# Optimization experiments

Hardware: AMD Instinct MI355X
Metric: run time of the kernel (lower is better)

## Reference

```python
import jax, jax.numpy as jnp
import numpy as np

N_HEADS = 16


def setup_inputs() -> dict:
    key = jax.random.key(0)
    ks = jax.random.split(key, 7)
    B, S, D = 2, 2048, 1024
    x = jax.random.normal(ks[0], (B, S, D), dtype=jnp.float32)
    attn_mask = jax.random.normal(ks[1], (S, S), dtype=jnp.float32) * 0.1
    attn_bias = jax.random.normal(ks[2], (B, S, S), dtype=jnp.float32) * 0.1
    Wqkv = jax.random.normal(ks[3], (D, 3 * D), dtype=jnp.float32) * (D ** -0.5)
    bqkv = jnp.zeros((3 * D,), dtype=jnp.float32)
    Wout = jax.random.normal(ks[4], (D, D), dtype=jnp.float32) * (D ** -0.5)
    bout = jnp.zeros((D,), dtype=jnp.float32)
    return {"x": x, "attn_mask": attn_mask, "attn_bias": attn_bias,
            "Wqkv": Wqkv, "bqkv": bqkv, "Wout": Wout, "bout": bout}


def reference(x, attn_mask, attn_bias, Wqkv, bqkv, Wout, bout):
    B, S, D = x.shape
    H = N_HEADS
    hd = D // H
    # qkv projection: [B,S,3D] -> [3,B,H,S,hd]
    qkv = (x @ Wqkv + bqkv).reshape(B, S, 3, H, hd).transpose(2, 0, 3, 1, 4)
    q, k, v = qkv[0], qkv[1], qkv[2]
    scores = jnp.einsum('bhqd,bhkd->bhqk', q, k) / (hd ** 0.5)
    scores = scores + attn_mask[None, None, :, :] + attn_bias[:, None, :, :]
    attn = jax.nn.softmax(scores, axis=-1)  # dropout p=0.0 (eval)
    out = jnp.einsum('bhqk,bhkd->bhqd', attn, v)
    out = out.transpose(0, 2, 1, 3).reshape(B, S, D)
    return out @ Wout + bout
```

## Files before the change

kernel.cpp:

```cpp
#include <hip/hip_runtime.h>
#include <hip/hip_bf16.h>


#define S_LEN 2048
#define DMODEL 1024
#define NH 16
#define HD 64

typedef __bf16 bf16x8 __attribute__((ext_vector_type(8)));
typedef __bf16 bf16x4 __attribute__((ext_vector_type(4)));
typedef __bf16 bf16x2v __attribute__((ext_vector_type(2)));
typedef float f32x4 __attribute__((ext_vector_type(4)));
typedef short s16x4 __attribute__((ext_vector_type(4)));

#define GLD_LDS16(g, l)                                              \
  __builtin_amdgcn_global_load_lds(                                  \
      (const __attribute__((address_space(1))) unsigned int*)(g),    \
      (__attribute__((address_space(3))) unsigned int*)(l), 16, 0, 0)

#if __has_builtin(__builtin_amdgcn_mfma_f32_16x16x16bf16_1k)
#define HAVE_MFMA_16x16x16_BF16 1
#else
#define HAVE_MFMA_16x16x16_BF16 0
#endif

#if __has_builtin(__builtin_amdgcn_exp2f)
#define EXP2F(x) __builtin_amdgcn_exp2f(x)
#else
static __device__ __forceinline__ float EXP2F(float x) {
  float r;
  asm volatile("v_exp_f32 %0, %1" : "=v"(r) : "v"(x));
  return r;
}
#endif

#define LOG2E 1.44269504f

__global__ __launch_bounds__(256) void preprocess(
    const float* __restrict__ x, const float* __restrict__ mask,
    const float* __restrict__ bias, const float* __restrict__ Wqkv,
    const float* __restrict__ Wout, __bf16* __restrict__ Xb,
    __bf16* __restrict__ Wt, __bf16* __restrict__ Wt2,
    __bf16* __restrict__ MB) {
  __shared__ __align__(16) char smem[64 * 65 * 4];
  const int bid = blockIdx.x;
  const int tid = threadIdx.x;

  if (bid < 4096) {
    int i = bid * 256 + tid;
    float4 v = ((const float4*)x)[i];
    bf16x4 o = {(__bf16)v.x, (__bf16)v.y, (__bf16)v.z, (__bf16)v.w};
    *(bf16x4*)&Xb[(size_t)i * 4] = o;
  } else if (bid < 5120) {
    const float* W;
    __bf16* Wo;
    int ncols, n0, k0;
    if (bid < 4864) {
      int id = bid - 4096;
      W = Wqkv; Wo = Wt; ncols = 3072;
      n0 = (id % 48) * 64; k0 = (id / 48) * 64;
    } else {
      int id = bid - 4864;
      W = Wout; Wo = Wt2; ncols = 1024;
      n0 = (id & 15) * 64; k0 = (id >> 4) * 64;
    }
    float(*tile)[65] = (float(*)[65])smem;
    {
      int c = tid & 63, r4 = tid >> 6;
#pragma unroll
      for (int p = 0; p < 16; ++p) {
        int r = r4 + p * 4;
        tile[r][c] = W[(size_t)(k0 + r) * ncols + n0 + c];
      }
    }
    __syncthreads();
    {
      int cc = (tid & 31) * 2, r8 = tid >> 5;
#pragma unroll
      for (int p = 0; p < 8; ++p) {
        int rr = r8 + p * 8;
        bf16x2v o = {(__bf16)tile[cc][rr], (__bf16)tile[cc + 1][rr]};
        *(bf16x2v*)&Wo[(size_t)(n0 + rr) * 1024 + k0 + cc] = o;
      }
    }
  } else {
    int id = bid - 5120;
    const int kt = id & 31, qt = (id >> 5) & 31, b = id >> 10;
    __bf16(*sm)[68] = (__bf16(*)[68])smem;
    {
      const int r0 = tid >> 4;
      const int cc = (tid & 15) * 4;
      const float* mrow = mask + (size_t)(qt * 64) * S_LEN + kt * 64;
      const float* brow =
          bias + ((size_t)b * S_LEN + qt * 64) * S_LEN + kt * 64;
#pragma unroll
      for (int p = 0; p < 4; ++p) {
        int r = r0 + p * 16;
        float4 m = *(const float4*)(mrow + (size_t)r * S_LEN + cc);
        float4 a = *(const float4*)(brow + (size_t)r * S_LEN + cc);
        sm[r][cc + 0] = (__bf16)((m.x + a.x) * LOG2E);
        sm[r][cc + 1] = (__bf16)((m.y + a.y) * LOG2E);
        sm[r][cc + 2] = (__bf16)((m.z + a.z) * LOG2E);
        sm[r][cc + 3] = (__bf16)((m.w + a.w) * LOG2E);
      }
    }
    __syncthreads();
    const int w = tid >> 6, lane = tid & 63;
    const int quad = lane >> 4, cl = lane & 15;
    __bf16 vals[16];
#pragma unroll
    for (int ct = 0; ct < 4; ++ct) {
      bf16x4 v = *(const bf16x4*)&sm[w * 16 + cl][ct * 16 + quad * 4];
      *(bf16x4*)&vals[ct * 4] = v;
    }
    __bf16* op =
        MB + (((size_t)(b * 32 + qt) * 32 + kt) * 4096) + (w * 64 + lane) * 16;
    *(bf16x8*)op = *(bf16x8*)&vals[0];
    *(bf16x8*)(op + 8) = *(bf16x8*)&vals[8];
  }
}

__global__ __launch_bounds__(256) void gemm_qkv_mfma(
    const __bf16* __restrict__ Xb, const __bf16* __restrict__ Wt,
    const float* __restrict__ bqkv, __bf16* __restrict__ Qb,
    __bf16* __restrict__ Kb, __bf16* __restrict__ Vtb) {
  __shared__ __align__(16) __bf16 As[128 * 32];
  __shared__ __align__(16) __bf16 Bs[128 * 32];
  const int tid = threadIdx.x;
  const int w = tid >> 6, lane = tid & 63;
  const int c = lane & 15, quad = lane >> 4;
  const int wm = w >> 1, wn = w & 1;
  const int rowBase = blockIdx.y * 128;
  const int colBase = blockIdx.x * 128;

  f32x4 acc[4][4] = {};

  const __bf16* gA0 =
      Xb + (size_t)(rowBase + w * 32 + (lane >> 2)) * 1024 + (lane & 3) * 8;
  const __bf16* gB0 =
      Wt + (size_t)(colBase + w * 32 + (lane >> 2)) * 1024 + (lane & 3) * 8;
  __bf16* lA0 = &As[(w * 32) * 32];
  __bf16* lB0 = &Bs[(w * 32) * 32];

  for (int k0 = 0; k0 < 1024; k0 += 32) {
    __syncthreads();
#pragma unroll
    for (int p = 0; p < 2; ++p) {
      GLD_LDS16(gA0 + (size_t)p * 16 * 1024 + k0, lA0 + p * 16 * 32);
      GLD_LDS16(gB0 + (size_t)p * 16 * 1024 + k0, lB0 + p * 16 * 32);
    }
    __syncthreads();

    bf16x8 af[4], bfr[4];
#pragma unroll
    for (int mt = 0; mt < 4; ++mt)
      af[mt] = *(const bf16x8*)&As[(wm * 64 + mt * 16 + c) * 32 + quad * 8];
#pragma unroll
    for (int nt = 0; nt < 4; ++nt)
      bfr[nt] = *(const bf16x8*)&Bs[(wn * 64 + nt * 16 + c) * 32 + quad * 8];
#pragma unroll
    for (int mt = 0; mt < 4; ++mt)
#pragma unroll
      for (int nt = 0; nt < 4; ++nt)
        acc[mt][nt] = __builtin_amdgcn_mfma_f32_16x16x32_bf16(
            af[mt], bfr[nt], acc[mt][nt], 0, 0, 0);
  }

#pragma unroll
  for (int mt = 0; mt < 4; ++mt) {
    int row0 = rowBase + wm * 64 + mt * 16 + quad * 4;
#pragma unroll
    for (int nt = 0; nt < 4; ++nt) {
      int col = colBase + wn * 64 + nt * 16 + c;
      float bias = bqkv[col];
      int three = col >> 10;
      int h = (col & 1023) >> 6;
      int d = col & 63;
#pragma unroll
      for (int r = 0; r < 4; ++r) {
        int rr = row0 + r;
        int bb = rr >> 11, s = rr & 2047;
        float val = acc[mt][nt][r] + bias;
        size_t ho = (size_t)(bb * NH + h);
        if (three == 0)
          Qb[(ho * S_LEN + s) * HD + d] = (__bf16)val;
        else if (three == 1)
          Kb[(ho * S_LEN + s) * HD + d] = (__bf16)val;
        else
          Vtb[(ho * HD + d) * S_LEN + s] = (__bf16)val;
      }
    }
  }
}

__global__ __launch_bounds__(256) void attn_mfma(
    const __bf16* __restrict__ Qb, const __bf16* __restrict__ Kb,
    const __bf16* __restrict__ Vtb, const __bf16* __restrict__ MB,
    __bf16* __restrict__ PO, float* __restrict__ L) {
  const int qt = blockIdx.x, h = blockIdx.y;
  const int b = blockIdx.z >> 1, half = blockIdx.z & 1;
  const int kt0 = half * 16;
  const int tid = threadIdx.x;
  const int w = tid >> 6;
  const int lane = tid & 63;
  const int c = lane & 15;
  const int quad = lane >> 4;

  __shared__ __align__(16) __bf16 Ks[2][64 * 64];
  __shared__ __align__(16) __bf16 Vs[2][64 * 64];
#if !HAVE_MFMA_16x16x16_BF16
  __shared__ __align__(16) __bf16 P2[4][16 * 72];
#endif

  const size_t headoff = (size_t)(b * NH + h) * S_LEN * HD;
  const __bf16* Qg = Qb + headoff + (size_t)(qt * 128) * HD;
  const __bf16* Kg = Kb + headoff;
  const __bf16* Vg = Vtb + headoff;
  const __bf16* MBq0 = MB + ((size_t)(b * 32 + qt * 2 + 0) * 32 + kt0) * 4096 +
                       (w * 64 + lane) * 16;
  const __bf16* MBq1 = MB + ((size_t)(b * 32 + qt * 2 + 1) * 32 + kt0) * 4096 +
                       (w * 64 + lane) * 16;

  __bf16* POx = PO + (size_t)half * 4194304;
  float* Lx = L + half * 65536;

  const int f0 = tid >> 3, f1 = f0 + 32;
  const int j = tid & 7;
  const int sj0 = j ^ (f0 & 7);
  const int sj1 = j ^ (f1 & 7);
  const int lds0 = tid * 8;
  const int lds1 = (256 + tid) * 8;

  bf16x8 qa[2][2];
#pragma unroll
  for (int g = 0; g < 2; ++g) {
    qa[g][0] = *(const bf16x8*)(Qg + (g * 64 + w * 16 + c) * HD + quad * 8);
    qa[g][1] =
        *(const bf16x8*)(Qg + (g * 64 + w * 16 + c) * HD + quad * 8 + 32);
  }

  const int rs0 = (quad ^ (c & 7)) * 8;
  const int rs1 = ((quad + 4) ^ (c & 7)) * 8;

  f32x4 Oa[2][4] = {};
  f32x4 psum[2] = {};

  const int kb0 = kt0 * 64;
  GLD_LDS16(Kg + (size_t)(kb0 + f0) * HD + sj0 * 8, &Ks[0][lds0]);
  GLD_LDS16(Kg + (size_t)(kb0 + f1) * HD + sj1 * 8, &Ks[0][lds1]);
  GLD_LDS16(Vg + (size_t)f0 * S_LEN + kb0 + sj0 * 8, &Vs[0][lds0]);
  GLD_LDS16(Vg + (size_t)f1 * S_LEN + kb0 + sj1 * 8, &Vs[0][lds1]);

  const __bf16* kgp0 = Kg + (size_t)(kb0 + 64 + f0) * HD + sj0 * 8;
  const __bf16* kgp1 = Kg + (size_t)(kb0 + 64 + f1) * HD + sj1 * 8;
  const __bf16* vgp0 = Vg + (size_t)f0 * S_LEN + kb0 + 64 + sj0 * 8;
  const __bf16* vgp1 = Vg + (size_t)f1 * S_LEN + kb0 + 64 + sj1 * 8;

  bf16x8 rMB[2][2];
  rMB[0][0] = *(const bf16x8*)MBq0;
  rMB[0][1] = *(const bf16x8*)(MBq0 + 8);
  rMB[1][0] = *(const bf16x8*)MBq1;
  rMB[1][1] = *(const bf16x8*)(MBq1 + 8);

  __syncthreads();

  const float c1 = 0.125f * LOG2E;

#pragma unroll 2
  for (int lkt = 0; lkt < 16; ++lkt) {
    const int cur = lkt & 1, nxt = cur ^ 1;
    bf16x8 nMB[2][2];
    {
      const __bf16* m0 = MBq0 + (size_t)(lkt + 1) * 4096;
      const __bf16* m1 = MBq1 + (size_t)(lkt + 1) * 4096;
      nMB[0][0] = *(const bf16x8*)m0;
      nMB[0][1] = *(const bf16x8*)(m0 + 8);
      nMB[1][0] = *(const bf16x8*)m1;
      nMB[1][1] = *(const bf16x8*)(m1 + 8);
    }
    if (lkt < 15) {
      GLD_LDS16(kgp0, &Ks[nxt][lds0]);
      GLD_LDS16(kgp1, &Ks[nxt][lds1]);
      GLD_LDS16(vgp0, &Vs[nxt][lds0]);
      GLD_LDS16(vgp1, &Vs[nxt][lds1]);
    }
    kgp0 += 64 * HD;
    kgp1 += 64 * HD;
    vgp0 += 64;
    vgp1 += 64;

    bf16x8 kf0[4], kf1[4];
#pragma unroll
    for (int ct = 0; ct < 4; ++ct) {
      kf0[ct] = *(const bf16x8*)&Ks[cur][(ct * 16 + c) * 64 + rs0];
      kf1[ct] = *(const bf16x8*)&Ks[cur][(ct * 16 + c) * 64 + rs1];
    }

    f32x4 sv[2][4];
    __builtin_amdgcn_s_setprio(1);
#pragma unroll
    for (int g = 0; g < 2; ++g)
#pragma unroll
      for (int ct = 0; ct < 4; ++ct) {
        f32x4 a = {};
        a = __builtin_amdgcn_mfma_f32_16x16x32_bf16(kf0[ct], qa[g][0], a, 0,
                                                    0, 0);
        a = __builtin_amdgcn_mfma_f32_16x16x32_bf16(kf1[ct], qa[g][1], a, 0,
                                                    0, 0);
        sv[g][ct] = a;
      }
    __builtin_amdgcn_s_setprio(0);

#if HAVE_MFMA_16x16x16_BF16
    s16x4 vf[4][4];
#pragma unroll
    for (int ft = 0; ft < 4; ++ft) {
      const int fr = ft * 16 + c;
#pragma unroll
      for (int ct = 0; ct < 4; ++ct) {
        const int chunk = ((ct * 2 + (quad >> 1)) ^ (fr & 7)) * 8 +
                          (quad & 1) * 4;
        vf[ft][ct] = *(const s16x4*)&Vs[cur][fr * 64 + chunk];
      }
    }
#endif

    s16x4 pb[2][4];
#pragma unroll
    for (int g = 0; g < 2; ++g)
#pragma unroll
      for (int ct = 0; ct < 4; ++ct) {
        f32x4 pv;
#pragma unroll
        for (int r = 0; r < 4; ++r) {
          float mb = (ct < 2) ? (float)rMB[g][0][ct * 4 + r]
                              : (float)rMB[g][1][(ct - 2) * 4 + r];
          pv[r] = EXP2F(sv[g][ct][r] * c1 + mb);
        }
        psum[g] += pv;
        __bf16 t4[4];
#pragma unroll
        for (int r = 0; r < 4; ++r) t4[r] = (__bf16)pv[r];
        pb[g][ct] = *(s16x4*)t4;
      }
#pragma unroll
    for (int g = 0; g < 2; ++g) {
      rMB[g][0] = nMB[g][0];
      rMB[g][1] = nMB[g][1];
    }

#if HAVE_MFMA_16x16x16_BF16
    __builtin_amdgcn_s_setprio(1);
#pragma unroll
    for (int g = 0; g < 2; ++g)
#pragma unroll
      for (int ft = 0; ft < 4; ++ft)
#pragma unroll
        for (int ct = 0; ct < 4; ++ct)
          Oa[g][ft] = __builtin_amdgcn_mfma_f32_16x16x16bf16_1k(
              vf[ft][ct], pb[g][ct], Oa[g][ft], 0, 0, 0);
    __builtin_amdgcn_s_setprio(0);
#else
#pragma unroll
    for (int g = 0; g < 2; ++g) {
#pragma unroll
      for (int ct = 0; ct < 4; ++ct)
        *(bf16x4*)&P2[w][c * 72 + ct * 16 + quad * 4] = *(bf16x4*)&pb[g][ct];
      bf16x8 pf0 = *(const bf16x8*)&P2[w][c * 72 + quad * 8];
      bf16x8 pf1 = *(const bf16x8*)&P2[w][c * 72 + 32 + quad * 8];
#pragma unroll
      for (int ft = 0; ft < 4; ++ft) {
        const int fr = ft * 16 + c;
        bf16x8 vf0 = *(const bf16x8*)&Vs[cur][fr * 64 + rs0];
        bf16x8 vf1 = *(const bf16x8*)&Vs[cur][fr * 64 + rs1];
        Oa[g][ft] = __builtin_amdgcn_mfma_f32_16x16x32_bf16(vf0, pf0,
                                                            Oa[g][ft], 0, 0, 0);
        Oa[g][ft] = __builtin_amdgcn_mfma_f32_16x16x32_bf16(vf1, pf1,
                                                            Oa[g][ft], 0, 0, 0);
      }
    }
#endif

    __syncthreads();
  }
#pragma unroll
  for (int g = 0; g < 2; ++g) {
    float lsum = psum[g][0] + psum[g][1] + psum[g][2] + psum[g][3];
    lsum += __shfl_xor(lsum, 16);
    lsum += __shfl_xor(lsum, 32);
    if (lane < 16)
      Lx[(size_t)(b * NH + h) * S_LEN + qt * 128 + g * 64 + w * 16 + c] = lsum;
    __bf16* orow = POx +
                   (size_t)(b * S_LEN + qt * 128 + g * 64 + w * 16 + c) *
                       DMODEL +
                   h * HD;
#pragma unroll
    for (int ft = 0; ft < 4; ++ft) {
      __bf16 t4[4];
#pragma unroll
      for (int r = 0; r < 4; ++r) t4[r] = (__bf16)Oa[g][ft][r];
      *(bf16x4*)(orow + ft * 16 + quad * 4) = *(bf16x4*)t4;
    }
  }
}

__global__ __launch_bounds__(256) void combine(const __bf16* __restrict__ PO,
                                               const float* __restrict__ L,
                                               __bf16* __restrict__ AOb) {
  const int i = blockIdx.x * 256 + threadIdx.x;
  const size_t e = (size_t)i * 8;
  const int hidx = (int)(e >> 6) & 15;
  const int s = (int)(e >> 10) & 2047;
  const int b = (int)(e >> 21);
  const size_t li = ((size_t)(b * NH + hidx) << 11) + s;
  const float invl = 1.0f / (L[li] + L[65536 + li]);
  bf16x8 a = *(const bf16x8*)&PO[e];
  bf16x8 c = *(const bf16x8*)&PO[4194304 + e];
  __bf16 o[8];
#pragma unroll
  for (int k = 0; k < 8; ++k)
    o[k] = (__bf16)(((float)a[k] + (float)c[k]) * invl);
  *(bf16x8*)&AOb[e] = *(bf16x8*)o;
}

__global__ __launch_bounds__(256) void gemm_out_mfma(
    const __bf16* __restrict__ AOb, const __bf16* __restrict__ Wt2,
    const float* __restrict__ bout, float* __restrict__ Out) {
  __shared__ __align__(16) __bf16 As[128 * 32];
  __shared__ __align__(16) __bf16 Bs[64 * 32];
  const int tid = threadIdx.x;
  const int w = tid >> 6, lane = tid & 63;
  const int c = lane & 15, quad = lane >> 4;
  const int rowBase = blockIdx.y * 128;
  const int colBase = blockIdx.x * 64;

  f32x4 acc[2][4] = {};

  const __bf16* gA0 =
      AOb + (size_t)(rowBase + w * 32 + (lane >> 2)) * 1024 + (lane & 3) * 8;
  const __bf16* gB0 =
      Wt2 + (size_t)(colBase + w * 16 + (lane >> 2)) * 1024 + (lane & 3) * 8;
  __bf16* lA0 = &As[(w * 32) * 32];
  __bf16* lB0 = &Bs[(w * 16) * 32];

  for (int k0 = 0; k0 < 1024; k0 += 32) {
    __syncthreads();
#pragma unroll
    for (int p = 0; p < 2; ++p)
      GLD_LDS16(gA0 + (size_t)p * 16 * 1024 + k0, lA0 + p * 16 * 32);
    GLD_LDS16(gB0 + k0, lB0);
    __syncthreads();

    bf16x8 af[2], bfr[4];
#pragma unroll
    for (int mt = 0; mt < 2; ++mt)
      af[mt] = *(const bf16x8*)&As[(w * 32 + mt * 16 + c) * 32 + quad * 8];
#pragma unroll
    for (int nt = 0; nt < 4; ++nt)
      bfr[nt] = *(const bf16x8*)&Bs[(nt * 16 + c) * 32 + quad * 8];
#pragma unroll
    for (int mt = 0; mt < 2; ++mt)
#pragma unroll
      for (int nt = 0; nt < 4; ++nt)
        acc[mt][nt] = __builtin_amdgcn_mfma_f32_16x16x32_bf16(
            af[mt], bfr[nt], acc[mt][nt], 0, 0, 0);
  }

#pragma unroll
  for (int mt = 0; mt < 2; ++mt) {
    int row0 = rowBase + w * 32 + mt * 16 + quad * 4;
#pragma unroll
    for (int nt = 0; nt < 4; ++nt) {
      int col = colBase + nt * 16 + c;
      float bias = bout[col];
#pragma unroll
      for (int r = 0; r < 4; ++r)
        Out[(size_t)(row0 + r) * 1024 + col] = acc[mt][nt][r] + bias;
    }
  }
}

extern "C" void kernel_launch(void* const* d_in, const int* in_sizes, int n_in,
                              void* d_out, int out_size, void* d_ws,
                              size_t ws_size, hipStream_t stream) {
  const float* x = (const float*)d_in[0];
  const float* attn_mask = (const float*)d_in[1];
  const float* attn_bias = (const float*)d_in[2];
  const float* Wqkv = (const float*)d_in[3];
  const float* bqkv = (const float*)d_in[4];
  const float* Wout = (const float*)d_in[5];
  const float* bout = (const float*)d_in[6];
  float* out = (float*)d_out;

  __bf16* base = (__bf16*)d_ws;
  __bf16* Xb = base;
  __bf16* PO = base;
  __bf16* Wt = base + 4194304;
  __bf16* Qb = base + 8388608;
  __bf16* Kb = base + 12582912;
  __bf16* Vtb = base + 16777216;
  __bf16* AOb = base + 16777216;
  __bf16* MB = base + 20971520;
  __bf16* Wt2 = base + 29360128;
  float* Lf = (float*)d_out;

  preprocess<<<7168, 256, 0, stream>>>(x, attn_mask, attn_bias, Wqkv, Wout,
                                       Xb, Wt, Wt2, MB);
  gemm_qkv_mfma<<<dim3(24, 32), 256, 0, stream>>>(Xb, Wt, bqkv, Qb, Kb, Vtb);
  attn_mfma<<<dim3(16, NH, 4), 256, 0, stream>>>(Qb, Kb, Vtb, MB, PO, Lf);
  combine<<<2048, 256, 0, stream>>>(PO, Lf, AOb);
  gemm_out_mfma<<<dim3(16, 32), 256, 0, stream>>>(AOb, Wt2, bout, out);
}
```

Before: 278.4 us.

## Drop split-K attention and combine kernel; process 128-key tiles per iteration

The attention kernel no longer splits the key range into two halves. Each block now walks all 32 key tiles as 16 iterations of two 64-key subtiles, with doubled LDS staging, and normalizes the output itself, so the combine kernel and the partial-output/L buffers go away. The preprocess stage also loads each mask tile once and reuses it for both batches, which cuts mask reads and the block count. In exchange the attention grid halves to 512 blocks and LDS per block doubles, which lowers parallelism and occupancy on the GPU.

After: 270.8 us. -2.7%, faster.

```diff
diff --git a/kernel.cpp b/kernel.cpp
--- a/kernel.cpp
+++ b/kernel.cpp
@@ -85,38 +85,42 @@
     }
   } else {
     int id = bid - 5120;
-    const int kt = id & 31, qt = (id >> 5) & 31, b = id >> 10;
+    const int kt = id & 31, qt = id >> 5;
     __bf16(*sm)[68] = (__bf16(*)[68])smem;
-    {
-      const int r0 = tid >> 4;
-      const int cc = (tid & 15) * 4;
-      const float* mrow = mask + (size_t)(qt * 64) * S_LEN + kt * 64;
+    const int r0 = tid >> 4;
+    const int cc = (tid & 15) * 4;
+    const float* mrow = mask + (size_t)(qt * 64) * S_LEN + kt * 64;
+    float4 mld[4];
+#pragma unroll
+    for (int p = 0; p < 4; ++p)
+      mld[p] = *(const float4*)(mrow + (size_t)(r0 + p * 16) * S_LEN + cc);
+    const int w = tid >> 6, lane = tid & 63;
+    const int quad = lane >> 4, cl = lane & 15;
+    for (int b = 0; b < 2; ++b) {
       const float* brow =
           bias + ((size_t)b * S_LEN + qt * 64) * S_LEN + kt * 64;
 #pragma unroll
       for (int p = 0; p < 4; ++p) {
         int r = r0 + p * 16;
-        float4 m = *(const float4*)(mrow + (size_t)r * S_LEN + cc);
         float4 a = *(const float4*)(brow + (size_t)r * S_LEN + cc);
-        sm[r][cc + 0] = (__bf16)((m.x + a.x) * LOG2E);
-        sm[r][cc + 1] = (__bf16)((m.y + a.y) * LOG2E);
-        sm[r][cc + 2] = (__bf16)((m.z + a.z) * LOG2E);
-        sm[r][cc + 3] = (__bf16)((m.w + a.w) * LOG2E);
-      }
-    }
-    __syncthreads();
-    const int w = tid >> 6, lane = tid & 63;
-    const int quad = lane >> 4, cl = lane & 15;
-    __bf16 vals[16];
-#pragma unroll
-    for (int ct = 0; ct < 4; ++ct) {
-      bf16x4 v = *(const bf16x4*)&sm[w * 16 + cl][ct * 16 + quad * 4];
-      *(bf16x4*)&vals[ct * 4] = v;
-    }
-    __bf16* op =
-        MB + (((size_t)(b * 32 + qt) * 32 + kt) * 4096) + (w * 64 + lane) * 16;
-    *(bf16x8*)op = *(bf16x8*)&vals[0];
-    *(bf16x8*)(op + 8) = *(bf16x8*)&vals[8];
+        sm[r][cc + 0] = (__bf16)((mld[p].x + a.x) * LOG2E);
+        sm[r][cc + 1] = (__bf16)((mld[p].y + a.y) * LOG2E);
+        sm[r][cc + 2] = (__bf16)((mld[p].z + a.z) * LOG2E);
+        sm[r][cc + 3] = (__bf16)((mld[p].w + a.w) * LOG2E);
+      }
+      __syncthreads();
+      __bf16 vals[16];
+#pragma unroll
+      for (int ct = 0; ct < 4; ++ct) {
+        bf16x4 v = *(const bf16x4*)&sm[w * 16 + cl][ct * 16 + quad * 4];
+        *(bf16x4*)&vals[ct * 4] = v;
+      }
+      __bf16* op = MB + (((size_t)(b * 32 + qt) * 32 + kt) * 4096) +
+                   (w * 64 + lane) * 16;
+      *(bf16x8*)op = *(bf16x8*)&vals[0];
+      *(bf16x8*)(op + 8) = *(bf16x8*)&vals[8];
+      __syncthreads();
+    }
   }
 }
 
@@ -196,18 +200,16 @@
 __global__ __launch_bounds__(256) void attn_mfma(
     const __bf16* __restrict__ Qb, const __bf16* __restrict__ Kb,
     const __bf16* __restrict__ Vtb, const __bf16* __restrict__ MB,
-    __bf16* __restrict__ PO, float* __restrict__ L) {
-  const int qt = blockIdx.x, h = blockIdx.y;
-  const int b = blockIdx.z >> 1, half = blockIdx.z & 1;
-  const int kt0 = half * 16;
+    __bf16* __restrict__ AOb) {
+  const int qt = blockIdx.x, h = blockIdx.y, b = blockIdx.z;
   const int tid = threadIdx.x;
   const int w = tid >> 6;
   const int lane = tid & 63;
   const int c = lane & 15;
   const int quad = lane >> 4;
 
-  __shared__ __align__(16) __bf16 Ks[2][64 * 64];
-  __shared__ __align__(16) __bf16 Vs[2][64 * 64];
+  __shared__ __align__(16) __bf16 Ks[2][2][64 * 64];
+  __shared__ __align__(16) __bf16 Vs[2][2][64 * 64];
 #if !HAVE_MFMA_16x16x16_BF16
   __shared__ __align__(16) __bf16 P2[4][16 * 72];
 #endif
@@ -216,13 +218,10 @@
   const __bf16* Qg = Qb + headoff + (size_t)(qt * 128) * HD;
   const __bf16* Kg = Kb + headoff;
   const __bf16* Vg = Vtb + headoff;
-  const __bf16* MBq0 = MB + ((size_t)(b * 32 + qt * 2 + 0) * 32 + kt0) * 4096 +
-                       (w * 64 + lane) * 16;
-  const __bf16* MBq1 = MB + ((size_t)(b * 32 + qt * 2 + 1) * 32 + kt0) * 4096 +
-                       (w * 64 + lane) * 16;
-
-  __bf16* POx = PO + (size_t)half * 4194304;
-  float* Lx = L + half * 65536;
+  const __bf16* MBq0 =
+      MB + ((size_t)(b * 32 + qt * 2 + 0) * 32) * 4096 + (w * 64 + lane) * 16;
+  const __bf16* MBq1 =
+      MB + ((size_t)(b * 32 + qt * 2 + 1) * 32) * 4096 + (w * 64 + lane) * 16;
 
   const int f0 = tid >> 3, f1 = f0 + 32;
   const int j = tid & 7;
@@ -245,57 +244,16 @@
   f32x4 Oa[2][4] = {};
   f32x4 psum[2] = {};
 
-  const int kb0 = kt0 * 64;
-  GLD_LDS16(Kg + (size_t)(kb0 + f0) * HD + sj0 * 8, &Ks[0][lds0]);
-  GLD_LDS16(Kg + (size_t)(kb0 + f1) * HD + sj1 * 8, &Ks[0][lds1]);
-  GLD_LDS16(Vg + (size_t)f0 * S_LEN + kb0 + sj0 * 8, &Vs[0][lds0]);
-  GLD_LDS16(Vg + (size_t)f1 * S_LEN + kb0 + sj1 * 8, &Vs[0][lds1]);
-
-  const __bf16* kgp0 = Kg + (size_t)(kb0 + 64 + f0) * HD + sj0 * 8;
-  const __bf16* kgp1 = Kg + (size_t)(kb0 + 64 + f1) * HD + sj1 * 8;
-  const __bf16* vgp0 = Vg + (size_t)f0 * S_LEN + kb0 + 64 + sj0 * 8;
-  const __bf16* vgp1 = Vg + (size_t)f1 * S_LEN + kb0 + 64 + sj1 * 8;
-
-  bf16x8 rMB[2][2];
-  rMB[0][0] = *(const bf16x8*)MBq0;
-  rMB[0][1] = *(const bf16x8*)(MBq0 + 8);
-  rMB[1][0] = *(const bf16x8*)MBq1;
-  rMB[1][1] = *(const bf16x8*)(MBq1 + 8);
-
-  __syncthreads();
-
   const float c1 = 0.125f * LOG2E;
 
-#pragma unroll 2
-  for (int lkt = 0; lkt < 16; ++lkt) {
-    const int cur = lkt & 1, nxt = cur ^ 1;
-    bf16x8 nMB[2][2];
-    {
-      const __bf16* m0 = MBq0 + (size_t)(lkt + 1) * 4096;
-      const __bf16* m1 = MBq1 + (size_t)(lkt + 1) * 4096;
-      nMB[0][0] = *(const bf16x8*)m0;
-      nMB[0][1] = *(const bf16x8*)(m0 + 8);
-      nMB[1][0] = *(const bf16x8*)m1;
-      nMB[1][1] = *(const bf16x8*)(m1 + 8);
-    }
-    if (lkt < 15) {
-      GLD_LDS16(kgp0, &Ks[nxt][lds0]);
-      GLD_LDS16(kgp1, &Ks[nxt][lds1]);
-      GLD_LDS16(vgp0, &Vs[nxt][lds0]);
-      GLD_LDS16(vgp1, &Vs[nxt][lds1]);
-    }
-    kgp0 += 64 * HD;
-    kgp1 += 64 * HD;
-    vgp0 += 64;
-    vgp1 += 64;
-
+  auto subtile = [&](const __bf16* KsS, const __bf16* VsS,
+                     bf16x8(&rmb)[2][2]) {
     bf16x8 kf0[4], kf1[4];
 #pragma unroll
     for (int ct = 0; ct < 4; ++ct) {
-      kf0[ct] = *(const bf16x8*)&Ks[cur][(ct * 16 + c) * 64 + rs0];
-      kf1[ct] = *(const bf16x8*)&Ks[cur][(ct * 16 + c) * 64 + rs1];
-    }
-
+      kf0[ct] = *(const bf16x8*)&KsS[(ct * 16 + c) * 64 + rs0];
+      kf1[ct] = *(const bf16x8*)&KsS[(ct * 16 + c) * 64 + rs1];
+    }
     f32x4 sv[2][4];
     __builtin_amdgcn_s_setprio(1);
 #pragma unroll
@@ -320,7 +278,7 @@
       for (int ct = 0; ct < 4; ++ct) {
         const int chunk = ((ct * 2 + (quad >> 1)) ^ (fr & 7)) * 8 +
                           (quad & 1) * 4;
-        vf[ft][ct] = *(const s16x4*)&Vs[cur][fr * 64 + chunk];
+        vf[ft][ct] = *(const s16x4*)&VsS[fr * 64 + chunk];
       }
     }
 #endif
@@ -333,8 +291,8 @@
         f32x4 pv;
 #pragma unroll
         for (int r = 0; r < 4; ++r) {
-          float mb = (ct < 2) ? (float)rMB[g][0][ct * 4 + r]
-                              : (float)rMB[g][1][(ct - 2) * 4 + r];
+          float mb = (ct < 2) ? (float)rmb[g][0][ct * 4 + r]
+                              : (float)rmb[g][1][(ct - 2) * 4 + r];
           pv[r] = EXP2F(sv[g][ct][r] * c1 + mb);
         }
         psum[g] += pv;
@@ -343,11 +301,6 @@
         for (int r = 0; r < 4; ++r) t4[r] = (__bf16)pv[r];
         pb[g][ct] = *(s16x4*)t4;
       }
-#pragma unroll
-    for (int g = 0; g < 2; ++g) {
-      rMB[g][0] = nMB[g][0];
-      rMB[g][1] = nMB[g][1];
-    }
 
 #if HAVE_MFMA_16x16x16_BF16
     __builtin_amdgcn_s_setprio(1);
@@ -371,8 +324,8 @@
 #pragma unroll
       for (int ft = 0; ft < 4; ++ft) {
         const int fr = ft * 16 + c;
-        bf16x8 vf0 = *(const bf16x8*)&Vs[cur][fr * 64 + rs0];
-        bf16x8 vf1 = *(const bf16x8*)&Vs[cur][fr * 64 + rs1];
+        bf16x8 vf0 = *(const bf16x8*)&VsS[fr * 64 + rs0];
+        bf16x8 vf1 = *(const bf16x8*)&VsS[fr * 64 + rs1];
         Oa[g][ft] = __builtin_amdgcn_mfma_f32_16x16x32_bf16(vf0, pf0,
                                                             Oa[g][ft], 0, 0, 0);
         Oa[g][ft] = __builtin_amdgcn_mfma_f32_16x16x32_bf16(vf1, pf1,
@@ -380,17 +333,88 @@
       }
     }
 #endif
+  };
+
+  GLD_LDS16(Kg + (size_t)f0 * HD + sj0 * 8, &Ks[0][0][lds0]);
+  GLD_LDS16(Kg + (size_t)f1 * HD + sj1 * 8, &Ks[0][0][lds1]);
+  GLD_LDS16(Kg + (size_t)(64 + f0) * HD + sj0 * 8, &Ks[0][1][lds0]);
+  GLD_LDS16(Kg + (size_t)(64 + f1) * HD + sj1 * 8, &Ks[0][1][lds1]);
+  GLD_LDS16(Vg + (size_t)f0 * S_LEN + sj0 * 8, &Vs[0][0][lds0]);
+  GLD_LDS16(Vg + (size_t)f1 * S_LEN + sj1 * 8, &Vs[0][0][lds1]);
+  GLD_LDS16(Vg + (size_t)f0 * S_LEN + 64 + sj0 * 8, &Vs[0][1][lds0]);
+  GLD_LDS16(Vg + (size_t)f1 * S_LEN + 64 + sj1 * 8, &Vs[0][1][lds1]);
+
+  const __bf16* kgp0 = Kg + (size_t)(128 + f0) * HD + sj0 * 8;
+  const __bf16* kgp1 = Kg + (size_t)(128 + f1) * HD + sj1 * 8;
+  const __bf16* vgp0 = Vg + (size_t)f0 * S_LEN + 128 + sj0 * 8;
+  const __bf16* vgp1 = Vg + (size_t)f1 * S_LEN + 128 + sj1 * 8;
+
+  bf16x8 rMBA[2][2], rMBB[2][2];
+  rMBA[0][0] = *(const bf16x8*)MBq0;
+  rMBA[0][1] = *(const bf16x8*)(MBq0 + 8);
+  rMBA[1][0] = *(const bf16x8*)MBq1;
+  rMBA[1][1] = *(const bf16x8*)(MBq1 + 8);
+  rMBB[0][0] = *(const bf16x8*)(MBq0 + 4096);
+  rMBB[0][1] = *(const bf16x8*)(MBq0 + 4096 + 8);
+  rMBB[1][0] = *(const bf16x8*)(MBq1 + 4096);
+  rMBB[1][1] = *(const bf16x8*)(MBq1 + 4096 + 8);
+
+  __syncthreads();
+
+#pragma unroll 2
+  for (int t = 0; t < 16; ++t) {
+    const int cur = t & 1, nxt = cur ^ 1;
+    if (t < 15) {
+      GLD_LDS16(kgp0, &Ks[nxt][0][lds0]);
+      GLD_LDS16(kgp1, &Ks[nxt][0][lds1]);
+      GLD_LDS16(kgp0 + 64 * HD, &Ks[nxt][1][lds0]);
+      GLD_LDS16(kgp1 + 64 * HD, &Ks[nxt][1][lds1]);
+      GLD_LDS16(vgp0, &Vs[nxt][0][lds0]);
+      GLD_LDS16(vgp1, &Vs[nxt][0][lds1]);
+      GLD_LDS16(vgp0 + 64, &Vs[nxt][1][lds0]);
+      GLD_LDS16(vgp1 + 64, &Vs[nxt][1][lds1]);
+    }
+    kgp0 += 128 * HD;
+    kgp1 += 128 * HD;
+    vgp0 += 128;
+    vgp1 += 128;
+
+    subtile(&Ks[cur][0][0], &Vs[cur][0][0], rMBA);
+
+    bf16x8 nMBA[2][2], nMBB[2][2];
+    {
+      const __bf16* m0 = MBq0 + (size_t)(2 * t + 2) * 4096;
+      const __bf16* m1 = MBq1 + (size_t)(2 * t + 2) * 4096;
+      nMBA[0][0] = *(const bf16x8*)m0;
+      nMBA[0][1] = *(const bf16x8*)(m0 + 8);
+      nMBA[1][0] = *(const bf16x8*)m1;
+      nMBA[1][1] = *(const bf16x8*)(m1 + 8);
+      nMBB[0][0] = *(const bf16x8*)(m0 + 4096);
+      nMBB[0][1] = *(const bf16x8*)(m0 + 4096 + 8);
+      nMBB[1][0] = *(const bf16x8*)(m1 + 4096);
+      nMBB[1][1] = *(const bf16x8*)(m1 + 4096 + 8);
+    }
+
+    subtile(&Ks[cur][1][0], &Vs[cur][1][0], rMBB);
+
+#pragma unroll
+    for (int g = 0; g < 2; ++g) {
+      rMBA[g][0] = nMBA[g][0];
+      rMBA[g][1] = nMBA[g][1];
+      rMBB[g][0] = nMBB[g][0];
+      rMBB[g][1] = nMBB[g][1];
+    }
 
     __syncthreads();
   }
+
 #pragma unroll
   for (int g = 0; g < 2; ++g) {
     float lsum = psum[g][0] + psum[g][1] + psum[g][2] + psum[g][3];
     lsum += __shfl_xor(lsum, 16);
     lsum += __shfl_xor(lsum, 32);
-    if (lane < 16)
-      Lx[(size_t)(b * NH + h) * S_LEN + qt * 128 + g * 64 + w * 16 + c] = lsum;
-    __bf16* orow = POx +
+    const float invl = 1.0f / lsum;
+    __bf16* orow = AOb +
                    (size_t)(b * S_LEN + qt * 128 + g * 64 + w * 16 + c) *
                        DMODEL +
                    h * HD;
@@ -398,29 +422,10 @@
     for (int ft = 0; ft < 4; ++ft) {
       __bf16 t4[4];
 #pragma unroll
-      for (int r = 0; r < 4; ++r) t4[r] = (__bf16)Oa[g][ft][r];
+      for (int r = 0; r < 4; ++r) t4[r] = (__bf16)(Oa[g][ft][r] * invl);
       *(bf16x4*)(orow + ft * 16 + quad * 4) = *(bf16x4*)t4;
     }
   }
-}
-
-__global__ __launch_bounds__(256) void combine(const __bf16* __restrict__ PO,
-                                               const float* __restrict__ L,
-                                               __bf16* __restrict__ AOb) {
-  const int i = blockIdx.x * 256 + threadIdx.x;
-  const size_t e = (size_t)i * 8;
-  const int hidx = (int)(e >> 6) & 15;
-  const int s = (int)(e >> 10) & 2047;
-  const int b = (int)(e >> 21);
-  const size_t li = ((size_t)(b * NH + hidx) << 11) + s;
-  const float invl = 1.0f / (L[li] + L[65536 + li]);
-  bf16x8 a = *(const bf16x8*)&PO[e];
-  bf16x8 c = *(const bf16x8*)&PO[4194304 + e];
-  __bf16 o[8];
-#pragma unroll
-  for (int k = 0; k < 8; ++k)
-    o[k] = (__bf16)(((float)a[k] + (float)c[k]) * invl);
-  *(bf16x8*)&AOb[e] = *(bf16x8*)o;
 }
 
 __global__ __launch_bounds__(256) void gemm_out_mfma(
@@ -494,20 +499,17 @@
 
   __bf16* base = (__bf16*)d_ws;
   __bf16* Xb = base;
-  __bf16* PO = base;
+  __bf16* AOb = base;
   __bf16* Wt = base + 4194304;
   __bf16* Qb = base + 8388608;
   __bf16* Kb = base + 12582912;
   __bf16* Vtb = base + 16777216;
-  __bf16* AOb = base + 16777216;
   __bf16* MB = base + 20971520;
   __bf16* Wt2 = base + 29360128;
-  float* Lf = (float*)d_out;
-
-  preprocess<<<7168, 256, 0, stream>>>(x, attn_mask, attn_bias, Wqkv, Wout,
+
+  preprocess<<<6144, 256, 0, stream>>>(x, attn_mask, attn_bias, Wqkv, Wout,
                                        Xb, Wt, Wt2, MB);
   gemm_qkv_mfma<<<dim3(24, 32), 256, 0, stream>>>(Xb, Wt, bqkv, Qb, Kb, Vtb);
-  attn_mfma<<<dim3(16, NH, 4), 256, 0, stream>>>(Qb, Kb, Vtb, MB, PO, Lf);
-  combine<<<2048, 256, 0, stream>>>(PO, Lf, AOb);
+  attn_mfma<<<dim3(16, NH, 2), 256, 0, stream>>>(Qb, Kb, Vtb, MB, AOb);
   gemm_out_mfma<<<dim3(16, 32), 256, 0, stream>>>(AOb, Wt2, bout, out);
 }
```
